# Optimization experiments

Hardware: AMD Instinct MI355X
Metric: run time of the kernel (lower is better)

The kernel has to match this reference:

```python
import jax, jax.numpy as jnp
import numpy as np

NF, B, C, H, W = 5, 8, 64, 128, 128

def setup_inputs() -> dict:
    key = jax.random.key(0)
    k1, k2, k3, k4, k5 = jax.random.split(key, 5)
    return {
        "inp": jax.random.normal(k1, (NF, B, C, H, W), dtype=jnp.float32),
        "origin_w": jax.random.normal(k2, (C, NF * C), dtype=jnp.float32) * 0.05,
        "origin_b": jax.random.normal(k3, (C,), dtype=jnp.float32) * 0.05,
        "out_w": jax.random.normal(k4, (1, 2 * C), dtype=jnp.float32) * 0.05,
        "out_b": jax.random.normal(k5, (1,), dtype=jnp.float32) * 0.05,
    }

def reference(inp, origin_w, origin_b, out_w, out_b):
    nf, b, c, h, w = inp.shape
    # concat frames along channel dim: [b, nf*c, h, w]
    x = jnp.transpose(inp, (1, 0, 2, 3, 4)).reshape(b, nf * c, h, w)
    # 1x1 conv -> origin query, viewed as [b, c, 1, h*w]
    origin = jnp.einsum('ok,bkhw->bohw', origin_w, x) + origin_b[None, :, None, None]
    origin = origin.reshape(b, c, 1, h * w)
    last = inp[-1]  # [b, c, h, w]
    # difference basis: [b, c, nf-1, h*w]
    basis = jnp.stack([last - inp[i] for i in range(nf - 1)], axis=2).reshape(b, c, nf - 1, h * w)
    # L2 normalize over the spatial (last) dim, torch F.normalize semantics (eps=1e-12)
    norm = jnp.sqrt(jnp.sum(basis * basis, axis=-1, keepdims=True))
    basis1 = basis / jnp.maximum(norm, 1e-12)
    # tiny-MN batched matmuls: [b,c,1,hw] x [b,c,hw,nf-1] -> [b,c,1,nf-1]
    score = jnp.einsum('bcik,bcjk->bcij', origin, basis1)
    # [b,c,1,nf-1] x [b,c,nf-1,hw] -> [b,c,1,hw]; original views back as (b,c,w,h)
    out = jnp.einsum('bcij,bcjk->bcik', score, basis1).reshape(b, c, w, h)
    cat = jnp.concatenate([out, last], axis=1)  # [b, 2c, h, w]
    y = jnp.einsum('ok,bkhw->bohw', out_w, cat) + out_b[None, :, None, None]
    return y
```

## Files before the change

kernel.cpp:

```cpp
#include <hip/hip_runtime.h>
#include <math.h>

#define NF 5
#define NB 8
#define NC 64
#define HW 16384
#define NK 320
#define EN_FLOATS (NB*NC*8)

#define WIN1 256
#define NT  40

__device__ __forceinline__ float redsum64(float v){
#pragma unroll
    for (int m = 1; m < 64; m <<= 1) v += __shfl_xor(v, m, 64);
    return v;
}

__global__ __launch_bounds__(256, 4) void k1_fused(
    const float* __restrict__ inp, const float* __restrict__ Wg,
    const float* __restrict__ bias, float* __restrict__ EN)
{
    __shared__ float S[2*8*WIN1];

    const int tid = threadIdx.x;
    const int l    = tid & 63;
    const int wv   = __builtin_amdgcn_readfirstlane(tid >> 6);
    const int blk  = blockIdx.x;
    const int xcd  = blk & 7;
    const int q    = blk >> 3;
    const int cgrp = q & 1;
    const int unit = xcd*64 + (q >> 1);
    const int b    = unit >> 6;
    const int s0   = (unit & 63) << 8;
    const int cf   = (cgrp << 5) + (wv << 3);
    const int srow = tid >> 5;
    const int scol = (tid & 31) << 2;

    float4 A[8];
    {
        float4 b0 = *reinterpret_cast<const float4*>(bias + cf);
        float4 b1 = *reinterpret_cast<const float4*>(bias + cf + 4);
        A[0] = make_float4(b0.x,b0.x,b0.x,b0.x);
        A[1] = make_float4(b0.y,b0.y,b0.y,b0.y);
        A[2] = make_float4(b0.z,b0.z,b0.z,b0.z);
        A[3] = make_float4(b0.w,b0.w,b0.w,b0.w);
        A[4] = make_float4(b1.x,b1.x,b1.x,b1.x);
        A[5] = make_float4(b1.y,b1.y,b1.y,b1.y);
        A[6] = make_float4(b1.z,b1.z,b1.z,b1.z);
        A[7] = make_float4(b1.w,b1.w,b1.w,b1.w);
    }

    const float* wbase = Wg + (size_t)cf*NK;

#define XROW(K) (inp + ((size_t)(((K)>>6)*NB + b)*NC + ((K)&63))*HW + s0 + scol)
#define LOADSET(R0,R1, KT) { const float* _p = XROW((KT)*8 + srow); \
    R0 = *reinterpret_cast<const float4*>(_p); \
    R1 = *reinterpret_cast<const float4*>(_p + 128); }
#define WRITESET(R0,R1, BUF) { float* _d = S + (BUF)*(8*WIN1) + srow*WIN1 + scol; \
    *reinterpret_cast<float4*>(_d)       = R0; \
    *reinterpret_cast<float4*>(_d + 128) = R1; }

    float4 rA0,rA1, rB0,rB1;
    LOADSET(rA0,rA1, 0)
    LOADSET(rB0,rB1, 1)
    WRITESET(rA0,rA1, 0)
    LOADSET(rA0,rA1, 2)
    __syncthreads();

#pragma unroll 2
    for (int kt=0; kt<NT; ++kt){
        if (kt & 1){
            if (kt < NT-1) WRITESET(rA0,rA1, (kt+1)&1)
            if (kt < NT-3) LOADSET (rA0,rA1, kt+3)
        } else {
            if (kt < NT-1) WRITESET(rB0,rB1, (kt+1)&1)
            if (kt < NT-3) LOADSET (rB0,rB1, kt+3)
        }
        const float* X  = S + (kt&1)*(8*WIN1) + (l<<2);
        const float* wt = wbase + kt*8;
#pragma unroll
        for (int k=0; k<8; ++k){
            float4 xv = *reinterpret_cast<const float4*>(X + k*WIN1);
#pragma unroll
            for (int j=0; j<8; ++j){
                float w = wt[(size_t)j*NK + k];
                A[j].x = fmaf(w, xv.x, A[j].x);
                A[j].y = fmaf(w, xv.y, A[j].y);
                A[j].z = fmaf(w, xv.z, A[j].z);
                A[j].w = fmaf(w, xv.w, A[j].w);
            }
        }
        __syncthreads();
    }
#undef LOADSET
#undef WRITESET
#undef XROW

#pragma unroll
    for (int j=0; j<8; ++j){
        const float* p4 = inp + ((size_t)(4*NB + b)*NC + (cf+j))*HW + s0 + (l<<2);
        float4 x4 = *reinterpret_cast<const float4*>(p4);
#pragma unroll
        for (int i=0; i<4; ++i){
            const float* pi = inp + ((size_t)(i*NB + b)*NC + (cf+j))*HW + s0 + (l<<2);
            float4 xi = *reinterpret_cast<const float4*>(pi);
            float dx = x4.x - xi.x, dy = x4.y - xi.y;
            float dz = x4.z - xi.z, dw = x4.w - xi.w;
            float n = fmaf(dx,dx, fmaf(dy,dy, fmaf(dz,dz, dw*dw)));
            float e = fmaf(A[j].x,dx, fmaf(A[j].y,dy, fmaf(A[j].z,dz, A[j].w*dw)));
            e = redsum64(e); n = redsum64(n);
            if (l == 0){
                float* p = EN + ((size_t)b*NC + cf + j)*8;
                atomicAdd(p + i,     e);
                atomicAdd(p + 4 + i, n);
            }
        }
    }
}

__global__ __launch_bounds__(256, 8) void k3_out(const float* __restrict__ inp,
        const float* __restrict__ EN, const float* __restrict__ out_w,
        const float* __restrict__ out_b, float* __restrict__ y)
{
    __shared__ float  Al[NK];
    __shared__ float4 P[256];
    const int tid = threadIdx.x;
    const int blk = blockIdx.x;
    const int b   = blk >> 7;
    const int s0  = (blk & 127) << 7;
    const int sg  = tid & 31;
    const int rg  = tid >> 5;

    if (tid < 64){
        const int c = tid;
        const float* e = EN + ((size_t)b*NC + c)*8;
        float w1 = out_w[c], w2 = out_w[NC + c];
        float csum = 0.f;
#pragma unroll
        for (int i=0; i<4; ++i){
            float nc = fmaxf(sqrtf(e[4+i]), 1e-12f);
            float coef = e[i] / (nc*nc);
            Al[i*NC + c] = -w1*coef;
            csum += coef;
        }
        Al[4*NC + c] = w1*csum + w2;
    }
    __syncthreads();

    float4 acc = make_float4(0.f,0.f,0.f,0.f);
    const int rbase = rg*40;
#pragma unroll 8
    for (int j=0; j<40; ++j){
        int r = rbase + j;
        const float* p = inp + ((size_t)((r>>6)*NB + b)*NC + (r&63))*HW + s0 + (sg<<2);
        float  w  = Al[r];
        float4 xv = *reinterpret_cast<const float4*>(p);
        acc.x = fmaf(w, xv.x, acc.x); acc.y = fmaf(w, xv.y, acc.y);
        acc.z = fmaf(w, xv.z, acc.z); acc.w = fmaf(w, xv.w, acc.w);
    }
    P[tid] = acc;
    __syncthreads();
    if (tid < 32){
        float4 r0 = P[tid];
        float vx = r0.x, vy = r0.y, vz = r0.z, vw = r0.w;
#pragma unroll
        for (int g=1; g<8; ++g){
            float4 q = P[tid + (g<<5)];
            vx += q.x; vy += q.y; vz += q.z; vw += q.w;
        }
        float bb = out_b[0];
        float4 o = make_float4(vx+bb, vy+bb, vz+bb, vw+bb);
        *reinterpret_cast<float4*>(y + (size_t)b*HW + s0 + (tid<<2)) = o;
    }
}

extern "C" void kernel_launch(void* const* d_in, const int* in_sizes, int n_in,
                              void* d_out, int out_size, void* d_ws, size_t ws_size,
                              hipStream_t stream)
{
    const float* inp      = (const float*)d_in[0];
    const float* origin_w = (const float*)d_in[1];
    const float* origin_b = (const float*)d_in[2];
    const float* out_w    = (const float*)d_in[3];
    const float* out_b    = (const float*)d_in[4];
    float* y  = (float*)d_out;
    float* EN = (float*)d_ws;

    hipMemsetAsync(EN, 0, EN_FLOATS*sizeof(float), stream);
    k1_fused<<<1024, 256, 0, stream>>>(inp, origin_w, origin_b, EN);
    k3_out  <<<1024, 256, 0, stream>>>(inp, EN, out_w, out_b, y);
}
```

Before: 308.7 us.

## Use 512-thread blocks covering all channels, prepack weights for vector loads

```diff
diff --git a/kernel.cpp b/kernel.cpp
--- a/kernel.cpp
+++ b/kernel.cpp
@@ -17,8 +17,17 @@
     return v;
 }
 
-__global__ __launch_bounds__(256, 4) void k1_fused(
-    const float* __restrict__ inp, const float* __restrict__ Wg,
+__global__ void k0_wp(const float* __restrict__ W, float* __restrict__ Wp){
+    int idx = blockIdx.x*256 + threadIdx.x;
+    if (idx < NC*NK){
+        int c = idx / NK;
+        int k = idx - c*NK;
+        Wp[(size_t)(c>>3)*(NK*8) + k*8 + (c&7)] = W[idx];
+    }
+}
+
+__global__ __launch_bounds__(512, 2) void k1_fused(
+    const float* __restrict__ inp, const float* __restrict__ Wp,
     const float* __restrict__ bias, float* __restrict__ EN)
 {
     __shared__ float S[2*8*WIN1];
@@ -27,15 +36,11 @@
     const int l    = tid & 63;
     const int wv   = __builtin_amdgcn_readfirstlane(tid >> 6);
     const int blk  = blockIdx.x;
-    const int xcd  = blk & 7;
-    const int q    = blk >> 3;
-    const int cgrp = q & 1;
-    const int unit = xcd*64 + (q >> 1);
-    const int b    = unit >> 6;
-    const int s0   = (unit & 63) << 8;
-    const int cf   = (cgrp << 5) + (wv << 3);
-    const int srow = tid >> 5;
-    const int scol = (tid & 31) << 2;
+    const int b    = blk >> 6;
+    const int s0   = (blk & 63) << 8;
+    const int cf   = wv << 3;
+    const int srow = tid >> 6;
+    const int scol = (tid & 63) << 2;
 
     float4 A[8];
     {
@@ -51,45 +56,51 @@
         A[7] = make_float4(b1.w,b1.w,b1.w,b1.w);
     }
 
-    const float* wbase = Wg + (size_t)cf*NK;
+    const float* Wk = Wp + (size_t)wv*(NK*8);
 
 #define XROW(K) (inp + ((size_t)(((K)>>6)*NB + b)*NC + ((K)&63))*HW + s0 + scol)
-#define LOADSET(R0,R1, KT) { const float* _p = XROW((KT)*8 + srow); \
-    R0 = *reinterpret_cast<const float4*>(_p); \
-    R1 = *reinterpret_cast<const float4*>(_p + 128); }
-#define WRITESET(R0,R1, BUF) { float* _d = S + (BUF)*(8*WIN1) + srow*WIN1 + scol; \
-    *reinterpret_cast<float4*>(_d)       = R0; \
-    *reinterpret_cast<float4*>(_d + 128) = R1; }
-
-    float4 rA0,rA1, rB0,rB1;
-    LOADSET(rA0,rA1, 0)
-    LOADSET(rB0,rB1, 1)
-    WRITESET(rA0,rA1, 0)
-    LOADSET(rA0,rA1, 2)
+#define LOADSET(R, KT)  { R = *reinterpret_cast<const float4*>(XROW((KT)*8 + srow)); }
+#define WRITESET(R, BUF){ *reinterpret_cast<float4*>(S + (BUF)*(8*WIN1) + srow*WIN1 + scol) = R; }
+
+    float4 rA, rB;
+    LOADSET(rA, 0)
+    LOADSET(rB, 1)
+    WRITESET(rA, 0)
+    LOADSET(rA, 2)
     __syncthreads();
 
 #pragma unroll 2
     for (int kt=0; kt<NT; ++kt){
         if (kt & 1){
-            if (kt < NT-1) WRITESET(rA0,rA1, (kt+1)&1)
-            if (kt < NT-3) LOADSET (rA0,rA1, kt+3)
+            if (kt < NT-1) WRITESET(rA, (kt+1)&1)
+            if (kt < NT-3) LOADSET (rA, kt+3)
         } else {
-            if (kt < NT-1) WRITESET(rB0,rB1, (kt+1)&1)
-            if (kt < NT-3) LOADSET (rB0,rB1, kt+3)
+            if (kt < NT-1) WRITESET(rB, (kt+1)&1)
+            if (kt < NT-3) LOADSET (rB, kt+3)
         }
         const float* X  = S + (kt&1)*(8*WIN1) + (l<<2);
-        const float* wt = wbase + kt*8;
+        const float* wt = Wk + kt*64;
 #pragma unroll
         for (int k=0; k<8; ++k){
             float4 xv = *reinterpret_cast<const float4*>(X + k*WIN1);
-#pragma unroll
-            for (int j=0; j<8; ++j){
-                float w = wt[(size_t)j*NK + k];
-                A[j].x = fmaf(w, xv.x, A[j].x);
-                A[j].y = fmaf(w, xv.y, A[j].y);
-                A[j].z = fmaf(w, xv.z, A[j].z);
-                A[j].w = fmaf(w, xv.w, A[j].w);
-            }
+            float4 w0 = *reinterpret_cast<const float4*>(wt + k*8);
+            float4 w1 = *reinterpret_cast<const float4*>(wt + k*8 + 4);
+            A[0].x = fmaf(w0.x, xv.x, A[0].x); A[0].y = fmaf(w0.x, xv.y, A[0].y);
+            A[0].z = fmaf(w0.x, xv.z, A[0].z); A[0].w = fmaf(w0.x, xv.w, A[0].w);
+            A[1].x = fmaf(w0.y, xv.x, A[1].x); A[1].y = fmaf(w0.y, xv.y, A[1].y);
+            A[1].z = fmaf(w0.y, xv.z, A[1].z); A[1].w = fmaf(w0.y, xv.w, A[1].w);
+            A[2].x = fmaf(w0.z, xv.x, A[2].x); A[2].y = fmaf(w0.z, xv.y, A[2].y);
+            A[2].z = fmaf(w0.z, xv.z, A[2].z); A[2].w = fmaf(w0.z, xv.w, A[2].w);
+            A[3].x = fmaf(w0.w, xv.x, A[3].x); A[3].y = fmaf(w0.w, xv.y, A[3].y);
+            A[3].z = fmaf(w0.w, xv.z, A[3].z); A[3].w = fmaf(w0.w, xv.w, A[3].w);
+            A[4].x = fmaf(w1.x, xv.x, A[4].x); A[4].y = fmaf(w1.x, xv.y, A[4].y);
+            A[4].z = fmaf(w1.x, xv.z, A[4].z); A[4].w = fmaf(w1.x, xv.w, A[4].w);
+            A[5].x = fmaf(w1.y, xv.x, A[5].x); A[5].y = fmaf(w1.y, xv.y, A[5].y);
+            A[5].z = fmaf(w1.y, xv.z, A[5].z); A[5].w = fmaf(w1.y, xv.w, A[5].w);
+            A[6].x = fmaf(w1.z, xv.x, A[6].x); A[6].y = fmaf(w1.z, xv.y, A[6].y);
+            A[6].z = fmaf(w1.z, xv.z, A[6].z); A[6].w = fmaf(w1.z, xv.w, A[6].w);
+            A[7].x = fmaf(w1.w, xv.x, A[7].x); A[7].y = fmaf(w1.w, xv.y, A[7].y);
+            A[7].z = fmaf(w1.w, xv.z, A[7].z); A[7].w = fmaf(w1.w, xv.w, A[7].w);
         }
         __syncthreads();
     }
@@ -127,10 +138,10 @@
     __shared__ float4 P[256];
     const int tid = threadIdx.x;
     const int blk = blockIdx.x;
-    const int b   = blk >> 7;
-    const int s0  = (blk & 127) << 7;
-    const int sg  = tid & 31;
-    const int rg  = tid >> 5;
+    const int b   = blk >> 6;
+    const int s0  = (blk & 63) << 8;
+    const int sg  = tid & 63;
+    const int rg  = tid >> 6;
 
     if (tid < 64){
         const int c = tid;
@@ -149,9 +160,9 @@
     __syncthreads();
 
     float4 acc = make_float4(0.f,0.f,0.f,0.f);
-    const int rbase = rg*40;
+    const int rbase = rg*80;
 #pragma unroll 8
-    for (int j=0; j<40; ++j){
+    for (int j=0; j<80; ++j){
         int r = rbase + j;
         const float* p = inp + ((size_t)((r>>6)*NB + b)*NC + (r&63))*HW + s0 + (sg<<2);
         float  w  = Al[r];
@@ -161,16 +172,13 @@
     }
     P[tid] = acc;
     __syncthreads();
-    if (tid < 32){
-        float4 r0 = P[tid];
-        float vx = r0.x, vy = r0.y, vz = r0.z, vw = r0.w;
-#pragma unroll
-        for (int g=1; g<8; ++g){
-            float4 q = P[tid + (g<<5)];
-            vx += q.x; vy += q.y; vz += q.z; vw += q.w;
-        }
+    if (tid < 64){
+        float4 r0 = P[tid], r1 = P[tid+64], r2 = P[tid+128], r3 = P[tid+192];
         float bb = out_b[0];
-        float4 o = make_float4(vx+bb, vy+bb, vz+bb, vw+bb);
+        float4 o = make_float4(r0.x+r1.x+r2.x+r3.x + bb,
+                               r0.y+r1.y+r2.y+r3.y + bb,
+                               r0.z+r1.z+r2.z+r3.z + bb,
+                               r0.w+r1.w+r2.w+r3.w + bb);
         *reinterpret_cast<float4*>(y + (size_t)b*HW + s0 + (tid<<2)) = o;
     }
 }
@@ -185,9 +193,13 @@
     const float* out_w    = (const float*)d_in[3];
     const float* out_b    = (const float*)d_in[4];
     float* y  = (float*)d_out;
-    float* EN = (float*)d_ws;
+    float* ws = (float*)d_ws;
+
+    float* EN = ws;
+    float* Wp = ws + EN_FLOATS;
 
     hipMemsetAsync(EN, 0, EN_FLOATS*sizeof(float), stream);
-    k1_fused<<<1024, 256, 0, stream>>>(inp, origin_w, origin_b, EN);
-    k3_out  <<<1024, 256, 0, stream>>>(inp, EN, out_w, out_b, y);
-}
+    k0_wp   <<<80,  256, 0, stream>>>(origin_w, Wp);
+    k1_fused<<<512, 512, 0, stream>>>(inp, Wp, origin_b, EN);
+    k3_out  <<<512, 256, 0, stream>>>(inp, EN, out_w, out_b, y);
+}
```

Result: slower. 321.2 us (+4.0%).
